# Kernel tuning notes

Hardware: AMD Instinct MI355X
Metric: run time of the kernel (lower is better)

Reference implementation:

```python
import jax, jax.numpy as jnp
from jax import lax
import numpy as np

EPS = 4e-3            # geoopt float32 ball boundary eps
MAXNORM = 1.0 - EPS   # c = 1 Poincare ball


def _norm(x):
    return jnp.sqrt(jnp.maximum(jnp.sum(x * x, axis=-1, keepdims=True), 1e-15))


def expmap0(u):
    n = _norm(u)
    return jnp.tanh(n) * u / n


def projx(x):
    n = _norm(x)
    return jnp.where(n > MAXNORM, x * (MAXNORM / n), x)


def mobius_add(x, y):
    x2 = jnp.sum(x * x, -1, keepdims=True)
    y2 = jnp.sum(y * y, -1, keepdims=True)
    xy = jnp.sum(x * y, -1, keepdims=True)
    num = (1.0 + 2.0 * xy + y2) * x + (1.0 - x2) * y
    den = 1.0 + 2.0 * xy + x2 * y2
    return num / jnp.maximum(den, 1e-15)


def mamba_layer(x, inW, convW, convb, xpW, dtW, dtb, A_log, Dp, outW):
    # x: [B,T,H]; inW: [2*Din,H]; convW: [Din,K]; xpW: [R+2N,Din]; dtW: [Din,R]
    B, T, H = x.shape
    Din, N = A_log.shape
    K = convW.shape[-1]
    R = dtW.shape[-1]
    xz = jnp.einsum('bth,dh->btd', x, inW)              # [B,T,2*Din]
    xr, z = jnp.split(xz, 2, axis=-1)
    xc = lax.conv_general_dilated(jnp.transpose(xr, (0, 2, 1)), convW[:, None, :],
                                  (1,), [(K - 1, 0)], feature_group_count=Din)
    u = jax.nn.silu(jnp.transpose(xc + convb[None, :, None], (0, 2, 1)))  # [B,T,Din]
    x_dbl = jnp.einsum('btd,ed->bte', u, xpW)           # [B,T,R+2N]
    dt_r, Bm, Cm = x_dbl[..., :R], x_dbl[..., R:R + N], x_dbl[..., R + N:]
    dt = jax.nn.softplus(jnp.einsum('btr,dr->btd', dt_r, dtW) + dtb)      # [B,T,Din]
    A = -jnp.exp(A_log)                                 # [Din,N]
    dA = jnp.exp(dt[..., None] * A)                     # [B,T,Din,N]
    dBu = dt[..., None] * Bm[:, :, None, :] * u[..., None]

    def step(h, ins):
        dA_t, dBu_t, C_t = ins
        h = dA_t * h + dBu_t                            # [B,Din,N]
        return h, jnp.einsum('bdn,bn->bd', h, C_t)

    h0 = jnp.zeros((B, Din, N), x.dtype)
    _, ys = lax.scan(step, h0, (jnp.moveaxis(dA, 1, 0), jnp.moveaxis(dBu, 1, 0), jnp.moveaxis(Cm, 1, 0)))
    y = jnp.moveaxis(ys, 0, 1) + Dp * u                 # [B,T,Din]
    return jnp.einsum('btd,hd->bth', y * jax.nn.silu(z), outW)


def _encode(xs, inp_W, inp_b, in_proj_W, conv_W, conv_b, xproj_W, dt_W, dt_b, A_log, D_skip, out_W, outp_W, outp_b):
    # xs: [4,B,T,1]; params carry leading branch dim 4, then layer dim 3
    def branch(x, iW, ib, ipW, cW, cb, xpW, dW, db, Al, Dp, oW, opW, opb):
        h = jnp.einsum('bti,hi->bth', x, iW) + ib
        for l in range(ipW.shape[0]):
            h = mamba_layer(h, ipW[l], cW[l], cb[l], xpW[l], dW[l], db[l], Al[l], Dp[l], oW[l])
        return jnp.tanh(jnp.einsum('bth,eh->bte', h, opW) + opb)
    return jax.vmap(branch)(xs, inp_W, inp_b, in_proj_W, conv_W, conv_b, xproj_W, dt_W, dt_b, A_log, D_skip, out_W, outp_W, outp_b)


def setup_inputs() -> dict:
    key = jax.random.key(0)
    ks = jax.random.split(key, 24)
    Br, B, T, H, Din, N, K, R, E, L = 4, 32, 1024, 64, 128, 16, 4, 4, 32, 3

    def rn(k, shape, s=0.05):
        return jax.random.normal(k, shape, jnp.float32) * s

    A_init = jnp.log(jnp.arange(1, N + 1, dtype=jnp.float32))
    return {
        'trend': jax.random.normal(ks[0], (B, T, 1), jnp.float32),
        'seasonal_weekly': jax.random.normal(ks[1], (B, T, 1), jnp.float32),
        'seasonal_daily': jax.random.normal(ks[2], (B, T, 1), jnp.float32),
        'residual': jax.random.normal(ks[3], (B, T, 1), jnp.float32),
        'inp_W': rn(ks[4], (Br, H, 1), 0.5),
        'inp_b': rn(ks[5], (Br, H)),
        'in_proj_W': rn(ks[6], (Br, L, 2 * Din, H)),
        'conv_W': rn(ks[7], (Br, L, Din, K), 0.2),
        'conv_b': rn(ks[8], (Br, L, Din)),
        'xproj_W': rn(ks[9], (Br, L, R + 2 * N, Din)),
        'dt_W': rn(ks[10], (Br, L, Din, R), 0.2),
        'dt_b': rn(ks[11], (Br, L, Din), 0.5) - 4.0,  # softplus(dt_b) small
        'A_log': jnp.tile(A_init, (Br, L, Din, 1)) + rn(ks[12], (Br, L, Din, N), 0.01),
        'D_skip': jnp.ones((Br, L, Din), jnp.float32) + rn(ks[13], (Br, L, Din), 0.01),
        'out_W': rn(ks[14], (Br, L, H, Din)),
        'outp_W': rn(ks[15], (Br, E, H)),
        'outp_b': rn(ks[16], (Br, E)),
    }


def reference(trend, seasonal_weekly, seasonal_daily, residual, inp_W, inp_b, in_proj_W, conv_W, conv_b, xproj_W, dt_W, dt_b, A_log, D_skip, out_W, outp_W, outp_b):
    xs = jnp.stack([trend, seasonal_weekly, seasonal_daily, residual], 0)  # [4,B,T,1]
    z = _encode(xs, inp_W, inp_b, in_proj_W, conv_W, conv_b, xproj_W, dt_W, dt_b, A_log, D_skip, out_W, outp_W, outp_b)  # [4,B,T,E]
    zh = projx(expmap0(z))
    t, w, d, r = zh[0], zh[1], zh[2], zh[3]
    comb = projx(mobius_add(mobius_add(t, mobius_add(w, d)), r))
    # stacked [trend_h, weekly_h, daily_h, residual_h, combined_h]
    return jnp.stack([t, w, d, r, comb], 0)
```

## Files before the change

### kernel.cpp

```cpp
#include <hip/hip_runtime.h>
#include <math.h>

#define TT 1024
#define DIN 128
#define HH 64
#define NN 16
#define EE 32
#define LL 3
#define BB 32

__device__ __forceinline__ float siluf(float x) { return x / (1.f + __expf(-x)); }

typedef __attribute__((ext_vector_type(8))) short bf16x8;
typedef __attribute__((ext_vector_type(4))) float f32x4;

__device__ __forceinline__ void split2(float x, ushort& hi, ushort& lo) {
  unsigned u = __float_as_uint(x);
  hi = (ushort)(u >> 16);
  float rem = x - __uint_as_float((u >> 16) << 16);
  lo = (ushort)(__float_as_uint(rem) >> 16);
}

#define FMA16(a, w) \
  acc[0][0] += a.x*w.x; acc[0][1] += a.x*w.y; acc[0][2] += a.x*w.z; acc[0][3] += a.x*w.w; \
  acc[1][0] += a.y*w.x; acc[1][1] += a.y*w.y; acc[1][2] += a.y*w.z; acc[1][3] += a.y*w.w; \
  acc[2][0] += a.z*w.x; acc[2][1] += a.z*w.y; acc[2][2] += a.z*w.z; acc[2][3] += a.z*w.w; \
  acc[3][0] += a.w*w.x; acc[3][1] += a.w*w.y; acc[3][2] += a.w*w.z; acc[3][3] += a.w*w.w;

__global__ __launch_bounds__(256) void k_xz(
    const float* __restrict__ x0, const float* __restrict__ x1,
    const float* __restrict__ x2, const float* __restrict__ x3,
    const float* __restrict__ h, const float* __restrict__ inprojW,
    const float* __restrict__ inpW, const float* __restrict__ inpb,
    float* __restrict__ xr, float* __restrict__ zb, int br0, int l) {
  __shared__ __align__(16) ushort Hh[64][72], Hl[64][72];
  __shared__ __align__(16) ushort Wh[64][72], Wl[64][72];
  const int tid = threadIdx.x;
  const int b  = blockIdx.y;
  const int t0 = blockIdx.x * 64;
  const int n0 = blockIdx.z * 64;
  const int br = br0 + (b >> 5);
  const float* Wg = inprojW + (size_t)((br * LL + l) * 2 * DIN + n0) * HH;
  const float* Hg = h + ((size_t)b * TT + t0) * HH;
  {
    int row = tid >> 2, c0 = (tid & 3) * 16;
    float xv = 0.f;
    if (l == 0) {
      int bb = b & 31;
      const float* xp = (br == 0) ? x0 : (br == 1) ? x1 : (br == 2) ? x2 : x3;
      xv = xp[bb * TT + t0 + row];
    }
    #pragma unroll
    for (int q = 0; q < 4; ++q) {
      float4 hv;
      if (l == 0) {
        float4 w4 = *(const float4*)(inpW + br * HH + c0 + q * 4);
        float4 b4 = *(const float4*)(inpb + br * HH + c0 + q * 4);
        hv.x = xv * w4.x + b4.x; hv.y = xv * w4.y + b4.y;
        hv.z = xv * w4.z + b4.z; hv.w = xv * w4.w + b4.w;
      } else {
        hv = *(const float4*)(Hg + (size_t)row * HH + c0 + q * 4);
      }
      ushort h0,h1,h2,h3,l0,l1,l2,l3;
      split2(hv.x,h0,l0); split2(hv.y,h1,l1); split2(hv.z,h2,l2); split2(hv.w,h3,l3);
      *(ushort4*)&Hh[row][c0 + q*4] = make_ushort4(h0,h1,h2,h3);
      *(ushort4*)&Hl[row][c0 + q*4] = make_ushort4(l0,l1,l2,l3);
      float4 wv = *(const float4*)(Wg + (size_t)row * HH + c0 + q * 4);
      split2(wv.x,h0,l0); split2(wv.y,h1,l1); split2(wv.z,h2,l2); split2(wv.w,h3,l3);
      *(ushort4*)&Wh[row][c0 + q*4] = make_ushort4(h0,h1,h2,h3);
      *(ushort4*)&Wl[row][c0 + q*4] = make_ushort4(l0,l1,l2,l3);
    }
  }
  __syncthreads();
  const int wave = tid >> 6, lane = tid & 63;
  const int quad = lane >> 4, l16 = lane & 15;
  const int nsub = (wave & 1) * 32, tsub = (wave >> 1) * 32;
  f32x4 acc[2][2] = {};
  #pragma unroll
  for (int k0 = 0; k0 < 64; k0 += 32) {
    bf16x8 Ah[2], Al[2], Bh[2], Bl[2];
    #pragma unroll
    for (int i = 0; i < 2; ++i) {
      Ah[i] = *(const bf16x8*)&Wh[nsub + i*16 + l16][k0 + quad*8];
      Al[i] = *(const bf16x8*)&Wl[nsub + i*16 + l16][k0 + quad*8];
      Bh[i] = *(const bf16x8*)&Hh[tsub + i*16 + l16][k0 + quad*8];
      Bl[i] = *(const bf16x8*)&Hl[tsub + i*16 + l16][k0 + quad*8];
    }
    #pragma unroll
    for (int i = 0; i < 2; ++i)
      #pragma unroll
      for (int j = 0; j < 2; ++j) {
        acc[i][j] = __builtin_amdgcn_mfma_f32_16x16x32_bf16(Ah[i], Bh[j], acc[i][j], 0, 0, 0);
        acc[i][j] = __builtin_amdgcn_mfma_f32_16x16x32_bf16(Ah[i], Bl[j], acc[i][j], 0, 0, 0);
        acc[i][j] = __builtin_amdgcn_mfma_f32_16x16x32_bf16(Al[i], Bh[j], acc[i][j], 0, 0, 0);
      }
  }
  #pragma unroll
  for (int i = 0; i < 2; ++i) {
    #pragma unroll
    for (int r = 0; r < 4; ++r) {
      int n = n0 + nsub + i*16 + quad*4 + r;
      float* dst = (n < DIN) ? (xr + ((size_t)b * DIN + n) * TT)
                             : (zb + ((size_t)b * DIN + (n - DIN)) * TT);
      #pragma unroll
      for (int j = 0; j < 2; ++j)
        dst[t0 + tsub + j*16 + l16] = acc[i][j][r];
    }
  }
}

__global__ __launch_bounds__(256) void k_xdbl(
    const float* __restrict__ xr, const float* __restrict__ convW,
    const float* __restrict__ convb, const float* __restrict__ xprojW,
    const float* __restrict__ dtW, const float* __restrict__ dtb,
    float* __restrict__ u, float* __restrict__ dt,
    float* __restrict__ Bm, float* __restrict__ Cm,
    int br0, int l) {
  __shared__ __align__(16) float Xr[16][72];
  __shared__ __align__(16) float As[16][68];
  __shared__ __align__(16) float Ws[16][44];
  __shared__ __align__(16) float Xs[40][68];
  const int tid = threadIdx.x;
  const int b  = blockIdx.y;
  const int t0 = blockIdx.x * 64;
  const int br = br0 + (b >> 5);
  const float* W = xprojW + (size_t)((br * LL + l) * 36) * DIN;
  float acc[4][4] = {};
  const int ti = tid & 15, ni = tid >> 4;
  const int rowk = tid >> 4, c4 = tid & 15;
  for (int k0 = 0; k0 < DIN; k0 += 16) {
    __syncthreads();
    {
      const float* src = xr + ((size_t)b * DIN + k0 + rowk) * TT + t0;
      *(float4*)&Xr[rowk][4 + c4 * 4] = *(const float4*)(src + c4 * 4);
      if (tid < 16) {
        float4 hv = make_float4(0.f, 0.f, 0.f, 0.f);
        if (t0 > 0) hv = *(const float4*)(xr + ((size_t)b * DIN + k0 + tid) * TT + t0 - 4);
        *(float4*)&Xr[tid][0] = hv;
      }
    }
    for (int idx = tid; idx < 640; idx += 256) {
      int jj = idx >> 4, kk = idx & 15;
      Ws[kk][jj] = (jj < 36) ? W[(size_t)jj * DIN + k0 + kk] : 0.f;
    }
    __syncthreads();
    {
      int d = k0 + rowk;
      const float* w = convW + (size_t)((br * LL + l) * DIN + d) * 4;
      float w0 = w[0], w1 = w[1], w2 = w[2], w3 = w[3];
      float cb = convb[(br * LL + l) * DIN + d];
      int i0 = c4 * 4;
      float o[4];
      #pragma unroll
      for (int q = 0; q < 4; ++q) {
        int j = i0 + q;
        float a = Xr[rowk][j+1]*w0 + Xr[rowk][j+2]*w1 + Xr[rowk][j+3]*w2 + Xr[rowk][j+4]*w3 + cb;
        o[q] = siluf(a);
      }
      float4 uo = make_float4(o[0], o[1], o[2], o[3]);
      *(float4*)&As[rowk][i0] = uo;
      *(float4*)(u + ((size_t)b * DIN + d) * TT + t0 + i0) = uo;
    }
    __syncthreads();
    if (ni < 10) {
      #pragma unroll
      for (int kk = 0; kk < 16; ++kk) {
        float4 a = *(const float4*)&As[kk][ti * 4];
        float4 w = *(const float4*)&Ws[kk][ni * 4];
        FMA16(a, w)
      }
    }
  }
  __syncthreads();
  if (ni < 10) {
    #pragma unroll
    for (int r = 0; r < 4; ++r)
      #pragma unroll
      for (int c = 0; c < 4; ++c)
        Xs[ni*4+c][ti*4+r] = acc[r][c];
  }
  __syncthreads();
  {
    int n = tid >> 4, i0 = (tid & 15) * 4;
    *(float4*)(Bm + ((size_t)b * NN + n) * TT + t0 + i0) = *(float4*)&Xs[4 + n][i0];
    *(float4*)(Cm + ((size_t)b * NN + n) * TT + t0 + i0) = *(float4*)&Xs[20 + n][i0];
  }
  {
    int d = tid >> 1, half = tid & 1;
    const float* wd = dtW + (size_t)((br * LL + l) * DIN + d) * 4;
    float w0 = wd[0], w1 = wd[1], w2 = wd[2], w3 = wd[3];
    float bias = dtb[(br * LL + l) * DIN + d];
    float* dtp = dt + ((size_t)b * DIN + d) * TT + t0 + half * 32;
    #pragma unroll
    for (int g8 = 0; g8 < 8; ++g8) {
      float o[4];
      #pragma unroll
      for (int q = 0; q < 4; ++q) {
        int i = half * 32 + g8 * 4 + q;
        float s = Xs[0][i]*w0 + Xs[1][i]*w1 + Xs[2][i]*w2 + Xs[3][i]*w3 + bias;
        float e = __expf(-fabsf(s));
        o[q] = fmaxf(s, 0.f) + __logf(1.f + e);
      }
      *(float4*)(dtp + g8*4) = make_float4(o[0], o[1], o[2], o[3]);
    }
  }
}

__global__ __launch_bounds__(256) void k_scan1(
    float* dtc, const float* __restrict__ u,
    const float* __restrict__ Bm, const float* __restrict__ Cm,
    const float* __restrict__ A_log, const float* __restrict__ D_skip,
    float* __restrict__ Hloc, float* __restrict__ g, int br0, int l) {
  __shared__ __align__(16) float Bl[16][68];
  __shared__ __align__(16) float Cl[16][68];
  const int bx  = blockIdx.x;
  const int b   = bx >> 5;
  const int rem = bx & 31;
  const int c   = rem >> 1;
  const int dh  = rem & 1;
  const int tid = threadIdx.x;
  {
    int row = tid >> 4, cc = (tid & 15) * 4;
    *(float4*)&Bl[row][cc] = *(const float4*)(Bm + ((size_t)b * NN + row) * TT + c * 64 + cc);
    *(float4*)&Cl[row][cc] = *(const float4*)(Cm + ((size_t)b * NN + row) * TT + c * 64 + cc);
  }
  __syncthreads();
  const int d  = dh * 64 + (tid >> 2);
  const int n0 = (tid & 3) * 4;
  const int br = br0 + (b >> 5);
  const int wbase = (br * LL + l) * DIN + d;
  float Ac[4];
  #pragma unroll
  for (int j = 0; j < 4; ++j) Ac[j] = -__expf(A_log[(size_t)wbase * NN + n0 + j]);
  float Dp = D_skip[wbase];
  float* dtp = dtc + ((size_t)b * DIN + d) * TT + c * 64;
  const float* up = u + ((size_t)b * DIN + d) * TT + c * 64;
  float* gp = g + ((size_t)b * DIN + d) * TT + c * 64;
  float hst[4] = {0.f, 0.f, 0.f, 0.f};
  float sd = 0.f;
  for (int t0 = 0; t0 < 64; t0 += 8) {
    float4 dq0 = *(const float4*)(dtp + t0);
    float4 dq1 = *(const float4*)(dtp + t0 + 4);
    float4 uq0 = *(const float4*)(up + t0);
    float4 uq1 = *(const float4*)(up + t0 + 4);
    float dts[8] = {dq0.x, dq0.y, dq0.z, dq0.w, dq1.x, dq1.y, dq1.z, dq1.w};
    float us[8]  = {uq0.x, uq0.y, uq0.z, uq0.w, uq1.x, uq1.y, uq1.z, uq1.w};
    float Bs[4][8], Cr[4][8];
    #pragma unroll
    for (int j = 0; j < 4; ++j) {
      float4 b0 = *(const float4*)&Bl[n0 + j][t0];
      float4 b1 = *(const float4*)&Bl[n0 + j][t0 + 4];
      Bs[j][0]=b0.x; Bs[j][1]=b0.y; Bs[j][2]=b0.z; Bs[j][3]=b0.w;
      Bs[j][4]=b1.x; Bs[j][5]=b1.y; Bs[j][6]=b1.z; Bs[j][7]=b1.w;
      float4 c0 = *(const float4*)&Cl[n0 + j][t0];
      float4 c1 = *(const float4*)&Cl[n0 + j][t0 + 4];
      Cr[j][0]=c0.x; Cr[j][1]=c0.y; Cr[j][2]=c0.z; Cr[j][3]=c0.w;
      Cr[j][4]=c1.x; Cr[j][5]=c1.y; Cr[j][6]=c1.z; Cr[j][7]=c1.w;
    }
    float yo[8], cd8[8];
    #pragma unroll
    for (int s = 0; s < 8; ++s) {
      float dtv = dts[s], uv = us[s];
      sd += dtv;
      cd8[s] = sd;
      float du = dtv * uv;
      float acc = 0.f;
      #pragma unroll
      for (int j = 0; j < 4; ++j) {
        float dA = __expf(dtv * Ac[j]);
        hst[j] = dA * hst[j] + du * Bs[j][s];
        acc += hst[j] * Cr[j][s];
      }
      acc += __shfl_xor(acc, 1, 4);
      acc += __shfl_xor(acc, 2, 4);
      yo[s] = acc + Dp * uv;
    }
    if ((tid & 3) == 0) {
      *(float4*)(gp + t0)      = make_float4(yo[0], yo[1], yo[2], yo[3]);
      *(float4*)(gp + t0 + 4)  = make_float4(yo[4], yo[5], yo[6], yo[7]);
      *(float4*)(dtp + t0)     = make_float4(cd8[0], cd8[1], cd8[2], cd8[3]);
      *(float4*)(dtp + t0 + 4) = make_float4(cd8[4], cd8[5], cd8[6], cd8[7]);
    }
  }
  *(float4*)(Hloc + (((size_t)b * DIN + d) * 16 + c) * 16 + n0) =
      make_float4(hst[0], hst[1], hst[2], hst[3]);
}

__global__ __launch_bounds__(256) void k_scan2(
    const float* __restrict__ cd, const float* __restrict__ Cm,
    const float* __restrict__ A_log, const float* __restrict__ Hloc,
    float* __restrict__ g, int br0, int l) {
  __shared__ __align__(16) float Cl[16][68];
  __shared__ __align__(16) float HinL[32][16];
  const int bx  = blockIdx.x;
  const int b   = bx >> 6;
  const int rem = bx & 63;
  const int c   = rem >> 2;
  const int dq  = rem & 3;
  const int tid = threadIdx.x;
  const int br  = br0 + (b >> 5);
  if (c == 0) return;
  {
    int row = tid >> 4, cc = (tid & 15) * 4;
    *(float4*)&Cl[row][cc] = *(const float4*)(Cm + ((size_t)b * NN + row) * TT + c * 64 + cc);
  }
  {
    int dloc = tid >> 3;
    int n0 = (tid & 7) * 2;
    int d = dq * 32 + dloc;
    int wbase = (br * LL + l) * DIN + d;
    float a0 = -__expf(A_log[(size_t)wbase * NN + n0]);
    float a1 = -__expf(A_log[(size_t)wbase * NN + n0 + 1]);
    float h0 = 0.f, h1 = 0.f;
    const float* cdrow = cd + ((size_t)b * DIN + d) * TT;
    const float* hlb = Hloc + ((size_t)b * DIN + d) * 256;
    for (int cc = 0; cc < c; ++cc) {
      float sdv = cdrow[cc * 64 + 63];
      float2 hl = *(const float2*)(hlb + cc * 16 + n0);
      h0 = __expf(a0 * sdv) * h0 + hl.x;
      h1 = __expf(a1 * sdv) * h1 + hl.y;
    }
    HinL[dloc][n0] = h0;
    HinL[dloc][n0 + 1] = h1;
  }
  __syncthreads();
  const int dloc = tid >> 3, tg = tid & 7;
  const int d  = dq * 32 + dloc;
  const float* al = A_log + (size_t)((br * LL + l) * DIN + d) * NN;
  float Ac16[16];
  #pragma unroll
  for (int n = 0; n < 16; ++n) Ac16[n] = -__expf(al[n]);
  size_t off = ((size_t)b * DIN + d) * TT + c * 64 + tg * 8;
  float4 cd0 = *(const float4*)(cd + off);
  float4 cd1 = *(const float4*)(cd + off + 4);
  float cd8[8] = {cd0.x, cd0.y, cd0.z, cd0.w, cd1.x, cd1.y, cd1.z, cd1.w};
  float* gp = g + off;
  float4 y0 = *(float4*)gp;
  float4 y1 = *(float4*)(gp + 4);
  float y8[8] = {y0.x, y0.y, y0.z, y0.w, y1.x, y1.y, y1.z, y1.w};
  const int tbase = tg * 8;
  #pragma unroll
  for (int n = 0; n < 16; ++n) {
    float hv = HinL[dloc][n];
    float an = Ac16[n];
    #pragma unroll
    for (int s = 0; s < 8; ++s)
      y8[s] += Cl[n][tbase + s] * __expf(an * cd8[s]) * hv;
  }
  *(float4*)gp       = make_float4(y8[0], y8[1], y8[2], y8[3]);
  *(float4*)(gp + 4) = make_float4(y8[4], y8[5], y8[6], y8[7]);
}

__global__ __launch_bounds__(256) void k_out(
    const float* __restrict__ graw, const float* __restrict__ zb,
    const float* __restrict__ outW, float* __restrict__ h, int br0, int l) {
  __shared__ __align__(16) ushort Ah_[64][72], Al_[64][72];
  __shared__ __align__(16) ushort Bh_[64][72], Bl_[64][72];
  const int tid = threadIdx.x;
  const int b  = blockIdx.y;
  const int t0 = blockIdx.x * 64;
  const int br = br0 + (b >> 5);
  const float* Wg = outW + (size_t)((br * LL + l) * HH) * DIN;
  const int wave = tid >> 6, lane = tid & 63;
  const int quad = lane >> 4, l16 = lane & 15;
  const int hsub = (wave & 1) * 32, tsub = (wave >> 1) * 32;
  f32x4 acc[2][2] = {};
  for (int k0 = 0; k0 < DIN; k0 += 64) {
    __syncthreads();
    {
      int row = tid >> 2, c0 = (tid & 3) * 16;
      #pragma unroll
      for (int q = 0; q < 4; ++q) {
        float4 wv = *(const float4*)(Wg + (size_t)row * DIN + k0 + c0 + q * 4);
        ushort h0,h1,h2,h3,l0,l1,l2,l3;
        split2(wv.x,h0,l0); split2(wv.y,h1,l1); split2(wv.z,h2,l2); split2(wv.w,h3,l3);
        *(ushort4*)&Ah_[row][c0 + q*4] = make_ushort4(h0,h1,h2,h3);
        *(ushort4*)&Al_[row][c0 + q*4] = make_ushort4(l0,l1,l2,l3);
        size_t off = ((size_t)b * DIN + k0 + row) * TT + t0 + c0 + q * 4;
        float4 gv = *(const float4*)(graw + off);
        float4 zv = *(const float4*)(zb + off);
        float a0 = gv.x * siluf(zv.x), a1 = gv.y * siluf(zv.y);
        float a2 = gv.z * siluf(zv.z), a3 = gv.w * siluf(zv.w);
        split2(a0,h0,l0); split2(a1,h1,l1); split2(a2,h2,l2); split2(a3,h3,l3);
        *(ushort4*)&Bh_[row][c0 + q*4] = make_ushort4(h0,h1,h2,h3);
        *(ushort4*)&Bl_[row][c0 + q*4] = make_ushort4(l0,l1,l2,l3);
      }
    }
    __syncthreads();
    #pragma unroll
    for (int kk = 0; kk < 64; kk += 32) {
      bf16x8 Ahf[2], Alf[2], Bhf[2], Blf[2];
      #pragma unroll
      for (int i = 0; i < 2; ++i) {
        Ahf[i] = *(const bf16x8*)&Ah_[hsub + i*16 + l16][kk + quad*8];
        Alf[i] = *(const bf16x8*)&Al_[hsub + i*16 + l16][kk + quad*8];
        Bhf[i] = *(const bf16x8*)&Bh_[tsub + i*16 + l16][kk + quad*8];
        Blf[i] = *(const bf16x8*)&Bl_[tsub + i*16 + l16][kk + quad*8];
      }
      #pragma unroll
      for (int i = 0; i < 2; ++i)
        #pragma unroll
        for (int j = 0; j < 2; ++j) {
          acc[i][j] = __builtin_amdgcn_mfma_f32_16x16x32_bf16(Ahf[i], Bhf[j], acc[i][j], 0, 0, 0);
          acc[i][j] = __builtin_amdgcn_mfma_f32_16x16x32_bf16(Ahf[i], Blf[j], acc[i][j], 0, 0, 0);
          acc[i][j] = __builtin_amdgcn_mfma_f32_16x16x32_bf16(Alf[i], Bhf[j], acc[i][j], 0, 0, 0);
        }
    }
  }
  #pragma unroll
  for (int i = 0; i < 2; ++i) {
    int hh0 = hsub + i*16 + quad*4;
    #pragma unroll
    for (int j = 0; j < 2; ++j) {
      int t = t0 + tsub + j*16 + l16;
      *(f32x4*)(h + ((size_t)b * TT + t) * HH + hh0) = acc[i][j];
    }
  }
}

__global__ __launch_bounds__(256) void k_ze(
    const float* __restrict__ h, const float* __restrict__ outpW,
    const float* __restrict__ outpb, float* __restrict__ ze, int br0) {
  __shared__ __align__(16) float As[16][132];
  __shared__ __align__(16) float Ws[16][36];
  __shared__ __align__(16) float Cs[128][36];
  const int tid = threadIdx.x;
  const int b  = blockIdx.y;
  const int t0 = blockIdx.x * 128;
  const int br = br0 + (b >> 5);
  const float* W = outpW + (size_t)br * EE * HH;
  float acc[4][4] = {};
  const int ti = tid & 31, ni = tid >> 5;
  for (int k0 = 0; k0 < HH; k0 += 16) {
    __syncthreads();
    {
      int i = tid >> 1, kq = (tid & 1) * 8;
      const float* src = h + ((size_t)b * TT + t0 + i) * HH + k0 + kq;
      float4 a0 = *(const float4*)src;
      float4 a1 = *(const float4*)(src + 4);
      As[kq+0][i]=a0.x; As[kq+1][i]=a0.y; As[kq+2][i]=a0.z; As[kq+3][i]=a0.w;
      As[kq+4][i]=a1.x; As[kq+5][i]=a1.y; As[kq+6][i]=a1.z; As[kq+7][i]=a1.w;
    }
    for (int idx = tid; idx < 512; idx += 256) {
      int jj = idx >> 4, kk = idx & 15;
      Ws[kk][jj] = W[(size_t)jj * HH + k0 + kk];
    }
    __syncthreads();
    #pragma unroll
    for (int kk = 0; kk < 16; ++kk) {
      float4 a = *(const float4*)&As[kk][ti * 4];
      float4 w = *(const float4*)&Ws[kk][ni * 4];
      FMA16(a, w)
    }
  }
  __syncthreads();
  float bj[4];
  #pragma unroll
  for (int c = 0; c < 4; ++c) bj[c] = outpb[br * EE + ni*4 + c];
  #pragma unroll
  for (int r = 0; r < 4; ++r)
    #pragma unroll
    for (int c = 0; c < 4; ++c)
      Cs[ti*4+r][ni*4+c] = tanhf(acc[r][c] + bj[c]);
  __syncthreads();
  int i = tid >> 1, j16 = (tid & 1) * 16;
  float* dst = ze + (((size_t)(br0 * 32 + b)) * TT + t0 + i) * EE + j16;
  #pragma unroll
  for (int q = 0; q < 4; ++q)
    *(float4*)(dst + q*4) = *(float4*)&Cs[i][j16 + q*4];
}

__device__ __forceinline__ void mobius_add32(const float* x, const float* y, float* o) {
  float x2 = 0.f, y2 = 0.f, xy = 0.f;
  #pragma unroll
  for (int i = 0; i < 32; ++i) { x2 += x[i]*x[i]; y2 += y[i]*y[i]; xy += x[i]*y[i]; }
  float ca  = 1.f + 2.f*xy + y2;
  float cb  = 1.f - x2;
  float den = 1.f + 2.f*xy + x2*y2;
  float inv = 1.f / fmaxf(den, 1e-15f);
  #pragma unroll
  for (int i = 0; i < 32; ++i) o[i] = (ca*x[i] + cb*y[i]) * inv;
}

__global__ __launch_bounds__(256) void k_hyper(const float* __restrict__ ze,
                                               float* __restrict__ out) {
  int idx = blockIdx.x * 256 + threadIdx.x;
  int b = idx >> 10, t = idx & 1023;
  float v[4][32];
  #pragma unroll
  for (int br = 0; br < 4; ++br) {
    const float* p = ze + (((size_t)br * BB + b) * TT + t) * EE;
    float s = 0.f;
    #pragma unroll
    for (int e = 0; e < 32; ++e) { v[br][e] = p[e]; s += v[br][e]*v[br][e]; }
    float nr = sqrtf(fmaxf(s, 1e-15f));
    float sc = tanhf(nr) / nr;
    float s2 = 0.f;
    #pragma unroll
    for (int e = 0; e < 32; ++e) { v[br][e] *= sc; s2 += v[br][e]*v[br][e]; }
    float n2 = sqrtf(fmaxf(s2, 1e-15f));
    if (n2 > 0.996f) {
      float sc2 = 0.996f / n2;
      #pragma unroll
      for (int e = 0; e < 32; ++e) v[br][e] *= sc2;
    }
    float* o = out + (((size_t)br * BB + b) * TT + t) * EE;
    #pragma unroll
    for (int e = 0; e < 32; ++e) o[e] = v[br][e];
  }
  float m1[32], m2[32];
  mobius_add32(v[1], v[2], m1);
  mobius_add32(v[0], m1, m2);
  mobius_add32(m2, v[3], m1);
  float s = 0.f;
  #pragma unroll
  for (int e = 0; e < 32; ++e) s += m1[e]*m1[e];
  float n = sqrtf(fmaxf(s, 1e-15f));
  if (n > 0.996f) {
    float sc = 0.996f / n;
    #pragma unroll
    for (int e = 0; e < 32; ++e) m1[e] *= sc;
  }
  float* o = out + (((size_t)4 * BB + b) * TT + t) * EE;
  #pragma unroll
  for (int e = 0; e < 32; ++e) o[e] = m1[e];
}

extern "C" void kernel_launch(void* const* d_in, const int* in_sizes, int n_in,
                              void* d_out, int out_size, void* d_ws, size_t ws_size,
                              hipStream_t stream) {
  const float* xs0 = (const float*)d_in[0];
  const float* xs1 = (const float*)d_in[1];
  const float* xs2 = (const float*)d_in[2];
  const float* xs3 = (const float*)d_in[3];
  const float* inpW   = (const float*)d_in[4];
  const float* inpb   = (const float*)d_in[5];
  const float* iprojW = (const float*)d_in[6];
  const float* convW  = (const float*)d_in[7];
  const float* convb  = (const float*)d_in[8];
  const float* xprojW = (const float*)d_in[9];
  const float* dtW    = (const float*)d_in[10];
  const float* dtb    = (const float*)d_in[11];
  const float* A_log  = (const float*)d_in[12];
  const float* D_skip = (const float*)d_in[13];
  const float* outW   = (const float*)d_in[14];
  const float* outpW  = (const float*)d_in[15];
  const float* outpb  = (const float*)d_in[16];
  float* out = (float*)d_out;
  float* ws  = (float*)d_ws;

  const size_t zeF = (size_t)4 * BB * TT * EE;
  const size_t perBl = 65536 + 4 * 131072 + 2 * 16384;
  auto needBytes = [&](int NB) { return (zeF + (size_t)NB * 32 * perBl) * 4; };
  int NB = 4;
  if (needBytes(4) > ws_size) NB = 2;
  if (NB == 2 && needBytes(2) > ws_size) NB = 1;
  const int nbl = NB * 32;

  float* ze = ws;
  float* h  = ze + zeF;
  float* xr = h  + (size_t)nbl * 65536;
  float* zb = xr + (size_t)nbl * 131072;
  float* u  = zb + (size_t)nbl * 131072;
  float* dt = u  + (size_t)nbl * 131072;
  float* Bm = dt + (size_t)nbl * 131072;
  float* Cm = Bm + (size_t)nbl * 16384;
  float* g  = xr;
  float* Hloc = h;

  for (int br0 = 0; br0 < 4; br0 += NB) {
    for (int l = 0; l < LL; ++l) {
      k_xz   <<<dim3(16, nbl, 4), 256, 0, stream>>>(xs0, xs1, xs2, xs3, h, iprojW,
                                                    inpW, inpb, xr, zb, br0, l);
      k_xdbl <<<dim3(16, nbl), 256, 0, stream>>>(xr, convW, convb, xprojW, dtW, dtb,
                                                 u, dt, Bm, Cm, br0, l);
      k_scan1<<<nbl * 32, 256, 0, stream>>>(dt, u, Bm, Cm, A_log, D_skip, Hloc, g, br0, l);
      k_scan2<<<nbl * 64, 256, 0, stream>>>(dt, Cm, A_log, Hloc, g, br0, l);
      k_out  <<<dim3(16, nbl), 256, 0, stream>>>(g, zb, outW, h, br0, l);
    }
    k_ze<<<dim3(8, nbl), 256, 0, stream>>>(h, outpW, outpb, ze, br0);
  }
  k_hyper<<<BB * TT / 256, 256, 0, stream>>>(ze, out);
}
```

Baseline: 1.128 ms.

## Fuse chunked-scan carry correction into output projection kernel

Removes the separate k_scan2 kernel and folds its work into k_out. Each k_out block first combines the per-chunk local states into the chunk's incoming state, then adds the carry correction to y while staging the gated activations for the MFMA GEMM. This drops one launch plus a read-modify-write pass over g. Hloc gets its own workspace region because k_out now writes h while still reading Hloc. The cost is more exp work and shared memory per k_out block, with fewer blocks doing the correction.

Result: slower. 1.270 ms (+12.6%).

```diff
diff --git a/kernel.cpp b/kernel.cpp
--- a/kernel.cpp
+++ b/kernel.cpp
@@ -286,81 +286,54 @@
       make_float4(hst[0], hst[1], hst[2], hst[3]);
 }
 
-__global__ __launch_bounds__(256) void k_scan2(
+__global__ __launch_bounds__(256) void k_out(
+    const float* __restrict__ graw, const float* __restrict__ zb,
+    const float* __restrict__ outW,
     const float* __restrict__ cd, const float* __restrict__ Cm,
     const float* __restrict__ A_log, const float* __restrict__ Hloc,
-    float* __restrict__ g, int br0, int l) {
-  __shared__ __align__(16) float Cl[16][68];
-  __shared__ __align__(16) float HinL[32][16];
-  const int bx  = blockIdx.x;
-  const int b   = bx >> 6;
-  const int rem = bx & 63;
-  const int c   = rem >> 2;
-  const int dq  = rem & 3;
-  const int tid = threadIdx.x;
-  const int br  = br0 + (b >> 5);
-  if (c == 0) return;
-  {
-    int row = tid >> 4, cc = (tid & 15) * 4;
-    *(float4*)&Cl[row][cc] = *(const float4*)(Cm + ((size_t)b * NN + row) * TT + c * 64 + cc);
-  }
-  {
-    int dloc = tid >> 3;
-    int n0 = (tid & 7) * 2;
-    int d = dq * 32 + dloc;
-    int wbase = (br * LL + l) * DIN + d;
-    float a0 = -__expf(A_log[(size_t)wbase * NN + n0]);
-    float a1 = -__expf(A_log[(size_t)wbase * NN + n0 + 1]);
-    float h0 = 0.f, h1 = 0.f;
-    const float* cdrow = cd + ((size_t)b * DIN + d) * TT;
-    const float* hlb = Hloc + ((size_t)b * DIN + d) * 256;
-    for (int cc = 0; cc < c; ++cc) {
-      float sdv = cdrow[cc * 64 + 63];
-      float2 hl = *(const float2*)(hlb + cc * 16 + n0);
-      h0 = __expf(a0 * sdv) * h0 + hl.x;
-      h1 = __expf(a1 * sdv) * h1 + hl.y;
-    }
-    HinL[dloc][n0] = h0;
-    HinL[dloc][n0 + 1] = h1;
-  }
-  __syncthreads();
-  const int dloc = tid >> 3, tg = tid & 7;
-  const int d  = dq * 32 + dloc;
-  const float* al = A_log + (size_t)((br * LL + l) * DIN + d) * NN;
-  float Ac16[16];
-  #pragma unroll
-  for (int n = 0; n < 16; ++n) Ac16[n] = -__expf(al[n]);
-  size_t off = ((size_t)b * DIN + d) * TT + c * 64 + tg * 8;
-  float4 cd0 = *(const float4*)(cd + off);
-  float4 cd1 = *(const float4*)(cd + off + 4);
-  float cd8[8] = {cd0.x, cd0.y, cd0.z, cd0.w, cd1.x, cd1.y, cd1.z, cd1.w};
-  float* gp = g + off;
-  float4 y0 = *(float4*)gp;
-  float4 y1 = *(float4*)(gp + 4);
-  float y8[8] = {y0.x, y0.y, y0.z, y0.w, y1.x, y1.y, y1.z, y1.w};
-  const int tbase = tg * 8;
-  #pragma unroll
-  for (int n = 0; n < 16; ++n) {
-    float hv = HinL[dloc][n];
-    float an = Ac16[n];
-    #pragma unroll
-    for (int s = 0; s < 8; ++s)
-      y8[s] += Cl[n][tbase + s] * __expf(an * cd8[s]) * hv;
-  }
-  *(float4*)gp       = make_float4(y8[0], y8[1], y8[2], y8[3]);
-  *(float4*)(gp + 4) = make_float4(y8[4], y8[5], y8[6], y8[7]);
-}
-
-__global__ __launch_bounds__(256) void k_out(
-    const float* __restrict__ graw, const float* __restrict__ zb,
-    const float* __restrict__ outW, float* __restrict__ h, int br0, int l) {
+    float* __restrict__ h, int br0, int l) {
   __shared__ __align__(16) ushort Ah_[64][72], Al_[64][72];
   __shared__ __align__(16) ushort Bh_[64][72], Bl_[64][72];
+  __shared__ __align__(16) float Cl[16][68];
+  __shared__ __align__(16) float HinL[128][16];
   const int tid = threadIdx.x;
   const int b  = blockIdx.y;
-  const int t0 = blockIdx.x * 64;
+  const int c  = blockIdx.x;
+  const int t0 = c * 64;
   const int br = br0 + (b >> 5);
   const float* Wg = outW + (size_t)((br * LL + l) * HH) * DIN;
+  if (c > 0) {
+    {
+      int row = tid >> 4, cc4 = (tid & 15) * 4;
+      *(float4*)&Cl[row][cc4] = *(const float4*)(Cm + ((size_t)b * NN + row) * TT + t0 + cc4);
+    }
+    {
+      int d = tid >> 1, n0 = (tid & 1) * 8;
+      int wbase = (br * LL + l) * DIN + d;
+      const float* al = A_log + (size_t)wbase * NN + n0;
+      float a[8];
+      #pragma unroll
+      for (int j = 0; j < 8; ++j) a[j] = -__expf(al[j]);
+      const float* cdrow = cd + ((size_t)b * DIN + d) * TT;
+      const float* hlb = Hloc + ((size_t)b * DIN + d) * 256;
+      float hc[8] = {0.f,0.f,0.f,0.f,0.f,0.f,0.f,0.f};
+      for (int cc = 0; cc < c; ++cc) {
+        float sdv = cdrow[cc * 64 + 63];
+        float4 h0 = *(const float4*)(hlb + cc * 16 + n0);
+        float4 h1 = *(const float4*)(hlb + cc * 16 + n0 + 4);
+        hc[0] = __expf(a[0]*sdv)*hc[0] + h0.x;
+        hc[1] = __expf(a[1]*sdv)*hc[1] + h0.y;
+        hc[2] = __expf(a[2]*sdv)*hc[2] + h0.z;
+        hc[3] = __expf(a[3]*sdv)*hc[3] + h0.w;
+        hc[4] = __expf(a[4]*sdv)*hc[4] + h1.x;
+        hc[5] = __expf(a[5]*sdv)*hc[5] + h1.y;
+        hc[6] = __expf(a[6]*sdv)*hc[6] + h1.z;
+        hc[7] = __expf(a[7]*sdv)*hc[7] + h1.w;
+      }
+      *(float4*)&HinL[d][n0]     = make_float4(hc[0], hc[1], hc[2], hc[3]);
+      *(float4*)&HinL[d][n0 + 4] = make_float4(hc[4], hc[5], hc[6], hc[7]);
+    }
+  }
   const int wave = tid >> 6, lane = tid & 63;
   const int quad = lane >> 4, l16 = lane & 15;
   const int hsub = (wave & 1) * 32, tsub = (wave >> 1) * 32;
@@ -369,6 +342,15 @@
     __syncthreads();
     {
       int row = tid >> 2, c0 = (tid & 3) * 16;
+      int d = k0 + row;
+      float Ac16[16], hin16[16];
+      if (c > 0) {
+        const float* al = A_log + (size_t)((br * LL + l) * DIN + d) * NN;
+        #pragma unroll
+        for (int n = 0; n < 16; ++n) Ac16[n] = -__expf(al[n]);
+        #pragma unroll
+        for (int n = 0; n < 16; ++n) hin16[n] = HinL[d][n];
+      }
       #pragma unroll
       for (int q = 0; q < 4; ++q) {
         float4 wv = *(const float4*)(Wg + (size_t)row * DIN + k0 + c0 + q * 4);
@@ -376,9 +358,23 @@
         split2(wv.x,h0,l0); split2(wv.y,h1,l1); split2(wv.z,h2,l2); split2(wv.w,h3,l3);
         *(ushort4*)&Ah_[row][c0 + q*4] = make_ushort4(h0,h1,h2,h3);
         *(ushort4*)&Al_[row][c0 + q*4] = make_ushort4(l0,l1,l2,l3);
-        size_t off = ((size_t)b * DIN + k0 + row) * TT + t0 + c0 + q * 4;
+        size_t off = ((size_t)b * DIN + d) * TT + t0 + c0 + q * 4;
         float4 gv = *(const float4*)(graw + off);
         float4 zv = *(const float4*)(zb + off);
+        if (c > 0) {
+          float4 cdv = *(const float4*)(cd + off);
+          float corr[4] = {0.f, 0.f, 0.f, 0.f};
+          int tb = c0 + q * 4;
+          #pragma unroll
+          for (int n = 0; n < 16; ++n) {
+            float w = hin16[n], an = Ac16[n];
+            corr[0] += Cl[n][tb+0] * __expf(an * cdv.x) * w;
+            corr[1] += Cl[n][tb+1] * __expf(an * cdv.y) * w;
+            corr[2] += Cl[n][tb+2] * __expf(an * cdv.z) * w;
+            corr[3] += Cl[n][tb+3] * __expf(an * cdv.w) * w;
+          }
+          gv.x += corr[0]; gv.y += corr[1]; gv.z += corr[2]; gv.w += corr[3];
+        }
         float a0 = gv.x * siluf(zv.x), a1 = gv.y * siluf(zv.y);
         float a2 = gv.z * siluf(zv.z), a3 = gv.w * siluf(zv.w);
         split2(a0,h0,l0); split2(a1,h1,l1); split2(a2,h2,l2); split2(a3,h3,l3);
@@ -550,7 +546,7 @@
   float* ws  = (float*)d_ws;
 
   const size_t zeF = (size_t)4 * BB * TT * EE;
-  const size_t perBl = 65536 + 4 * 131072 + 2 * 16384;
+  const size_t perBl = 65536 + 4 * 131072 + 2 * 16384 + 32768;
   auto needBytes = [&](int NB) { return (zeF + (size_t)NB * 32 * perBl) * 4; };
   int NB = 4;
   if (needBytes(4) > ws_size) NB = 2;
@@ -565,8 +561,8 @@
   float* dt = u  + (size_t)nbl * 131072;
   float* Bm = dt + (size_t)nbl * 131072;
   float* Cm = Bm + (size_t)nbl * 16384;
+  float* Hloc = Cm + (size_t)nbl * 16384;
   float* g  = xr;
-  float* Hloc = h;
 
   for (int br0 = 0; br0 < 4; br0 += NB) {
     for (int l = 0; l < LL; ++l) {
@@ -575,8 +571,8 @@
       k_xdbl <<<dim3(16, nbl), 256, 0, stream>>>(xr, convW, convb, xprojW, dtW, dtb,
                                                  u, dt, Bm, Cm, br0, l);
       k_scan1<<<nbl * 32, 256, 0, stream>>>(dt, u, Bm, Cm, A_log, D_skip, Hloc, g, br0, l);
-      k_scan2<<<nbl * 64, 256, 0, stream>>>(dt, Cm, A_log, Hloc, g, br0, l);
-      k_out  <<<dim3(16, nbl), 256, 0, stream>>>(g, zb, outW, h, br0, l);
+      k_out  <<<dim3(16, nbl), 256, 0, stream>>>(g, zb, outW, dt, Cm, A_log, Hloc,
+                                                 h, br0, l);
     }
     k_ze<<<dim3(8, nbl), 256, 0, stream>>>(h, outpW, outpb, ze, br0);
   }
```

## Fuse output projection into k_out and loop N-tiles inside k_xz

Applied to the files above, without the earlier changes.

k_xz now loops over the four 64-wide output tiles inside one block, so the H tile is loaded and split into bf16 hi/lo only once instead of once per z-block. The separate k_ze kernel is removed. On the last layer, k_out stages its result in shared memory (aliased onto the B buffers), then applies the E=32 projection, bias and tanh directly, skipping the h write and the re-read. The cost is a 4x smaller k_xz grid with serialized tiles, which lowers parallelism. The fused projection reads outpW directly from global memory for each thread.

Measured after the change: 1.186 ms. +5.1%, slower.

```diff
diff --git a/kernel.cpp b/kernel.cpp
--- a/kernel.cpp
+++ b/kernel.cpp
@@ -38,12 +38,10 @@
   const int tid = threadIdx.x;
   const int b  = blockIdx.y;
   const int t0 = blockIdx.x * 64;
-  const int n0 = blockIdx.z * 64;
   const int br = br0 + (b >> 5);
-  const float* Wg = inprojW + (size_t)((br * LL + l) * 2 * DIN + n0) * HH;
   const float* Hg = h + ((size_t)b * TT + t0) * HH;
+  const int row = tid >> 2, c0 = (tid & 3) * 16;
   {
-    int row = tid >> 2, c0 = (tid & 3) * 16;
     float xv = 0.f;
     if (l == 0) {
       int bb = b & 31;
@@ -65,47 +63,57 @@
       split2(hv.x,h0,l0); split2(hv.y,h1,l1); split2(hv.z,h2,l2); split2(hv.w,h3,l3);
       *(ushort4*)&Hh[row][c0 + q*4] = make_ushort4(h0,h1,h2,h3);
       *(ushort4*)&Hl[row][c0 + q*4] = make_ushort4(l0,l1,l2,l3);
-      float4 wv = *(const float4*)(Wg + (size_t)row * HH + c0 + q * 4);
-      split2(wv.x,h0,l0); split2(wv.y,h1,l1); split2(wv.z,h2,l2); split2(wv.w,h3,l3);
-      *(ushort4*)&Wh[row][c0 + q*4] = make_ushort4(h0,h1,h2,h3);
-      *(ushort4*)&Wl[row][c0 + q*4] = make_ushort4(l0,l1,l2,l3);
-    }
-  }
-  __syncthreads();
+    }
+  }
   const int wave = tid >> 6, lane = tid & 63;
   const int quad = lane >> 4, l16 = lane & 15;
   const int nsub = (wave & 1) * 32, tsub = (wave >> 1) * 32;
-  f32x4 acc[2][2] = {};
-  #pragma unroll
-  for (int k0 = 0; k0 < 64; k0 += 32) {
-    bf16x8 Ah[2], Al[2], Bh[2], Bl[2];
+  for (int n0 = 0; n0 < 2 * DIN; n0 += 64) {
+    const float* Wg = inprojW + (size_t)((br * LL + l) * 2 * DIN + n0) * HH;
+    {
+      #pragma unroll
+      for (int q = 0; q < 4; ++q) {
+        float4 wv = *(const float4*)(Wg + (size_t)row * HH + c0 + q * 4);
+        ushort h0,h1,h2,h3,l0,l1,l2,l3;
+        split2(wv.x,h0,l0); split2(wv.y,h1,l1); split2(wv.z,h2,l2); split2(wv.w,h3,l3);
+        *(ushort4*)&Wh[row][c0 + q*4] = make_ushort4(h0,h1,h2,h3);
+        *(ushort4*)&Wl[row][c0 + q*4] = make_ushort4(l0,l1,l2,l3);
+      }
+    }
+    __syncthreads();
+    f32x4 acc[2][2] = {};
+    #pragma unroll
+    for (int k0 = 0; k0 < 64; k0 += 32) {
+      bf16x8 Ah[2], Al[2], Bh[2], Bl[2];
+      #pragma unroll
+      for (int i = 0; i < 2; ++i) {
+        Ah[i] = *(const bf16x8*)&Wh[nsub + i*16 + l16][k0 + quad*8];
+        Al[i] = *(const bf16x8*)&Wl[nsub + i*16 + l16][k0 + quad*8];
+        Bh[i] = *(const bf16x8*)&Hh[tsub + i*16 + l16][k0 + quad*8];
+        Bl[i] = *(const bf16x8*)&Hl[tsub + i*16 + l16][k0 + quad*8];
+      }
+      #pragma unroll
+      for (int i = 0; i < 2; ++i)
+        #pragma unroll
+        for (int j = 0; j < 2; ++j) {
+          acc[i][j] = __builtin_amdgcn_mfma_f32_16x16x32_bf16(Ah[i], Bh[j], acc[i][j], 0, 0, 0);
+          acc[i][j] = __builtin_amdgcn_mfma_f32_16x16x32_bf16(Ah[i], Bl[j], acc[i][j], 0, 0, 0);
+          acc[i][j] = __builtin_amdgcn_mfma_f32_16x16x32_bf16(Al[i], Bh[j], acc[i][j], 0, 0, 0);
+        }
+    }
     #pragma unroll
     for (int i = 0; i < 2; ++i) {
-      Ah[i] = *(const bf16x8*)&Wh[nsub + i*16 + l16][k0 + quad*8];
-      Al[i] = *(const bf16x8*)&Wl[nsub + i*16 + l16][k0 + quad*8];
-      Bh[i] = *(const bf16x8*)&Hh[tsub + i*16 + l16][k0 + quad*8];
-      Bl[i] = *(const bf16x8*)&Hl[tsub + i*16 + l16][k0 + quad*8];
-    }
-    #pragma unroll
-    for (int i = 0; i < 2; ++i)
-      #pragma unroll
-      for (int j = 0; j < 2; ++j) {
-        acc[i][j] = __builtin_amdgcn_mfma_f32_16x16x32_bf16(Ah[i], Bh[j], acc[i][j], 0, 0, 0);
-        acc[i][j] = __builtin_amdgcn_mfma_f32_16x16x32_bf16(Ah[i], Bl[j], acc[i][j], 0, 0, 0);
-        acc[i][j] = __builtin_amdgcn_mfma_f32_16x16x32_bf16(Al[i], Bh[j], acc[i][j], 0, 0, 0);
-      }
-  }
-  #pragma unroll
-  for (int i = 0; i < 2; ++i) {
-    #pragma unroll
-    for (int r = 0; r < 4; ++r) {
-      int n = n0 + nsub + i*16 + quad*4 + r;
-      float* dst = (n < DIN) ? (xr + ((size_t)b * DIN + n) * TT)
-                             : (zb + ((size_t)b * DIN + (n - DIN)) * TT);
-      #pragma unroll
-      for (int j = 0; j < 2; ++j)
-        dst[t0 + tsub + j*16 + l16] = acc[i][j][r];
-    }
+      #pragma unroll
+      for (int r = 0; r < 4; ++r) {
+        int n = n0 + nsub + i*16 + quad*4 + r;
+        float* dst = (n < DIN) ? (xr + ((size_t)b * DIN + n) * TT)
+                               : (zb + ((size_t)b * DIN + (n - DIN)) * TT);
+        #pragma unroll
+        for (int j = 0; j < 2; ++j)
+          dst[t0 + tsub + j*16 + l16] = acc[i][j][r];
+      }
+    }
+    __syncthreads();
   }
 }
 
@@ -353,9 +361,14 @@
 
 __global__ __launch_bounds__(256) void k_out(
     const float* __restrict__ graw, const float* __restrict__ zb,
-    const float* __restrict__ outW, float* __restrict__ h, int br0, int l) {
+    const float* __restrict__ outW, const float* __restrict__ outpW,
+    const float* __restrict__ outpb, float* __restrict__ h,
+    float* __restrict__ ze, int br0, int l) {
   __shared__ __align__(16) ushort Ah_[64][72], Al_[64][72];
-  __shared__ __align__(16) ushort Bh_[64][72], Bl_[64][72];
+  __shared__ __align__(16) char smemB[2 * 64 * 72 * 2];
+  ushort (*Bh_)[72] = (ushort(*)[72])smemB;
+  ushort (*Bl_)[72] = (ushort(*)[72])(smemB + 64 * 72 * 2);
+  float  (*Hs)[68]  = (float(*)[68])smemB;
   const int tid = threadIdx.x;
   const int b  = blockIdx.y;
   const int t0 = blockIdx.x * 64;
@@ -407,67 +420,47 @@
         }
     }
   }
-  #pragma unroll
-  for (int i = 0; i < 2; ++i) {
-    int hh0 = hsub + i*16 + quad*4;
-    #pragma unroll
-    for (int j = 0; j < 2; ++j) {
-      int t = t0 + tsub + j*16 + l16;
-      *(f32x4*)(h + ((size_t)b * TT + t) * HH + hh0) = acc[i][j];
-    }
-  }
-}
-
-__global__ __launch_bounds__(256) void k_ze(
-    const float* __restrict__ h, const float* __restrict__ outpW,
-    const float* __restrict__ outpb, float* __restrict__ ze, int br0) {
-  __shared__ __align__(16) float As[16][132];
-  __shared__ __align__(16) float Ws[16][36];
-  __shared__ __align__(16) float Cs[128][36];
-  const int tid = threadIdx.x;
-  const int b  = blockIdx.y;
-  const int t0 = blockIdx.x * 128;
-  const int br = br0 + (b >> 5);
-  const float* W = outpW + (size_t)br * EE * HH;
-  float acc[4][4] = {};
-  const int ti = tid & 31, ni = tid >> 5;
-  for (int k0 = 0; k0 < HH; k0 += 16) {
-    __syncthreads();
-    {
-      int i = tid >> 1, kq = (tid & 1) * 8;
-      const float* src = h + ((size_t)b * TT + t0 + i) * HH + k0 + kq;
-      float4 a0 = *(const float4*)src;
-      float4 a1 = *(const float4*)(src + 4);
-      As[kq+0][i]=a0.x; As[kq+1][i]=a0.y; As[kq+2][i]=a0.z; As[kq+3][i]=a0.w;
-      As[kq+4][i]=a1.x; As[kq+5][i]=a1.y; As[kq+6][i]=a1.z; As[kq+7][i]=a1.w;
-    }
-    for (int idx = tid; idx < 512; idx += 256) {
-      int jj = idx >> 4, kk = idx & 15;
-      Ws[kk][jj] = W[(size_t)jj * HH + k0 + kk];
-    }
-    __syncthreads();
-    #pragma unroll
-    for (int kk = 0; kk < 16; ++kk) {
-      float4 a = *(const float4*)&As[kk][ti * 4];
-      float4 w = *(const float4*)&Ws[kk][ni * 4];
-      FMA16(a, w)
-    }
-  }
-  __syncthreads();
-  float bj[4];
-  #pragma unroll
-  for (int c = 0; c < 4; ++c) bj[c] = outpb[br * EE + ni*4 + c];
-  #pragma unroll
-  for (int r = 0; r < 4; ++r)
-    #pragma unroll
-    for (int c = 0; c < 4; ++c)
-      Cs[ti*4+r][ni*4+c] = tanhf(acc[r][c] + bj[c]);
-  __syncthreads();
-  int i = tid >> 1, j16 = (tid & 1) * 16;
-  float* dst = ze + (((size_t)(br0 * 32 + b)) * TT + t0 + i) * EE + j16;
-  #pragma unroll
-  for (int q = 0; q < 4; ++q)
-    *(float4*)(dst + q*4) = *(float4*)&Cs[i][j16 + q*4];
+  if (l != LL - 1) {
+    #pragma unroll
+    for (int i = 0; i < 2; ++i) {
+      int hh0 = hsub + i*16 + quad*4;
+      #pragma unroll
+      for (int j = 0; j < 2; ++j) {
+        int t = t0 + tsub + j*16 + l16;
+        *(f32x4*)(h + ((size_t)b * TT + t) * HH + hh0) = acc[i][j];
+      }
+    }
+  } else {
+    __syncthreads();
+    #pragma unroll
+    for (int i = 0; i < 2; ++i) {
+      int hh0 = hsub + i*16 + quad*4;
+      #pragma unroll
+      for (int j = 0; j < 2; ++j) {
+        int tl = tsub + j*16 + l16;
+        *(f32x4*)&Hs[tl][hh0] = acc[i][j];
+      }
+    }
+    __syncthreads();
+    const int tl = tid >> 2, e0 = (tid & 3) * 8;
+    const float* Wz = outpW + (size_t)br * EE * HH;
+    float o[8];
+    #pragma unroll
+    for (int e = 0; e < 8; ++e) {
+      const float* wrow = Wz + (size_t)(e0 + e) * HH;
+      float s = outpb[br * EE + e0 + e];
+      #pragma unroll
+      for (int hh = 0; hh < 64; hh += 4) {
+        float4 hv = *(const float4*)&Hs[tl][hh];
+        float4 wv = *(const float4*)(wrow + hh);
+        s += hv.x*wv.x + hv.y*wv.y + hv.z*wv.z + hv.w*wv.w;
+      }
+      o[e] = tanhf(s);
+    }
+    float* dst = ze + (((size_t)(br0 * 32 + b)) * TT + t0 + tl) * EE + e0;
+    *(float4*)dst       = make_float4(o[0], o[1], o[2], o[3]);
+    *(float4*)(dst + 4) = make_float4(o[4], o[5], o[6], o[7]);
+  }
 }
 
 __device__ __forceinline__ void mobius_add32(const float* x, const float* y, float* o) {
@@ -570,15 +563,15 @@
 
   for (int br0 = 0; br0 < 4; br0 += NB) {
     for (int l = 0; l < LL; ++l) {
-      k_xz   <<<dim3(16, nbl, 4), 256, 0, stream>>>(xs0, xs1, xs2, xs3, h, iprojW,
-                                                    inpW, inpb, xr, zb, br0, l);
+      k_xz   <<<dim3(16, nbl), 256, 0, stream>>>(xs0, xs1, xs2, xs3, h, iprojW,
+                                                 inpW, inpb, xr, zb, br0, l);
       k_xdbl <<<dim3(16, nbl), 256, 0, stream>>>(xr, convW, convb, xprojW, dtW, dtb,
                                                  u, dt, Bm, Cm, br0, l);
       k_scan1<<<nbl * 32, 256, 0, stream>>>(dt, u, Bm, Cm, A_log, D_skip, Hloc, g, br0, l);
       k_scan2<<<nbl * 64, 256, 0, stream>>>(dt, Cm, A_log, Hloc, g, br0, l);
-      k_out  <<<dim3(16, nbl), 256, 0, stream>>>(g, zb, outW, h, br0, l);
-    }
-    k_ze<<<dim3(8, nbl), 256, 0, stream>>>(h, outpW, outpb, ze, br0);
+      k_out  <<<dim3(16, nbl), 256, 0, stream>>>(g, zb, outW, outpW, outpb,
+                                                 h, ze, br0, l);
+    }
   }
   k_hyper<<<BB * TT / 256, 256, 0, stream>>>(ze, out);
 }
```
